# Optimization experiments

Hardware: AMD Instinct MI355X
Metric: run time of the kernel (lower is better)

## Reference

```python
import jax, jax.numpy as jnp
import numpy as np

TOP_K = 8  # config.top_k


def setup_inputs() -> dict:
    key = jax.random.key(0)
    k1, k2 = jax.random.split(key)
    B, S, H, E = 4, 4096, 4096, 64
    x = jax.random.normal(k1, (B, S, H), dtype=jnp.float32)
    # nn.Linear(hidden_size, expert_num, bias=False) weight: [E, H]
    W = jax.random.normal(k2, (E, H), dtype=jnp.float32) / np.sqrt(H).astype(np.float32)
    return {"x": x, "W": W}


def reference(x, W):
    # gate linear: [B,S,H] @ [E,H]^T -> [B,S,E]
    logits = jnp.einsum('bsh,eh->bse', x, W)
    # top-k along experts
    topk_vals, indices = jax.lax.top_k(logits, TOP_K)  # [B,S,K]
    # scatter topk values into a -inf-filled tensor. Since the scattered src
    # values are exactly the logits at those indices, this equals masking.
    E = logits.shape[-1]
    mask = jax.nn.one_hot(indices, E, dtype=bool).any(axis=-2)  # [B,S,E]
    sparse_logits = jnp.where(mask, logits, -jnp.inf)
    sparse_probs = jax.nn.softmax(sparse_logits, axis=-1)  # [B,S,E]
    gate_logit = logits.reshape(-1, E)  # [B*S, E]
    return sparse_probs, indices, gate_logit
```

## Files before the change

### kernel.cpp

```cpp
#include <hip/hip_runtime.h>
#include <math.h>

#define H_DIM  4096
#define E_NUM  64
#define N_TOK  16384
#define TPB    64
#define KC     64
#define NCHUNK (H_DIM / KC)
#define TOPK   8

#define N_PROBS  (N_TOK * E_NUM)
#define N_IDX    (N_TOK * TOPK)
#define OFF_IDX  N_PROBS
#define OFF_GATE (N_PROBS + N_IDX)


typedef __attribute__((ext_vector_type(8))) __fp16 half8;
typedef __attribute__((ext_vector_type(2))) __fp16 half2t;
typedef __attribute__((ext_vector_type(16))) float f32x16;
typedef __attribute__((ext_vector_type(4))) unsigned int uint4v;

#define XSCALE 64.0f
#define WSCALE 256.0f
#define DESCALE (1.0 / 16384.0)

__global__ __launch_bounds__(256, 1)
void gating_kernel(const float* __restrict__ x, const float* __restrict__ W,
                   float* __restrict__ out) {
  __shared__ union __align__(16) {
    struct { float xs[4][64][KC]; float ws[4][64][KC]; } t;
    float lg[TPB][E_NUM + 1];
  } u;

  const int tid  = threadIdx.x;
  const int tok0 = blockIdx.x * TPB;
  const int lane = tid & 63;
  const int wid  = tid >> 6;
  const int wm   = wid >> 1;
  const int wn   = wid & 1;
  const int l31  = lane & 31;
  const int arow = 32 * wm + l31;
  const int brow = 32 * wn + l31;
  const int khalf = 32 * (lane >> 5);

  const float* xg = x + (size_t)tok0 * H_DIM;

  auto stage = [&](const float* gbase, float* lds, int cbyte) {
#pragma unroll
    for (int i = 0; i < 4; ++i) {
      const int I   = wid * 4 + i;
      const int row = 4 * I + (lane >> 4);
      const int inrow = (lane & 15) * 16;
      const char* src = (const char*)(gbase + (size_t)row * H_DIM) + cbyte
                        + (inrow ^ ((row & 7) << 4));
      __builtin_amdgcn_global_load_lds(
          (const __attribute__((address_space(1))) unsigned int*)src,
          (__attribute__((address_space(3))) unsigned int*)((char*)lds + I * 1024),
          16, 0, 0);
    }
  };

  auto frag16 = [&](const float* base, int row, int q) -> float4 {
    return *(const float4*)((const char*)base + row * 256
                            + (q ^ ((row & 7) << 4)));
  };

  auto split8 = [&](float4 v0, float4 v1, float scale, half8& hi, half8& lo) {
    const float f[8] = {v0.x, v0.y, v0.z, v0.w, v1.x, v1.y, v1.z, v1.w};
    unsigned hu[4], lu[4];
#pragma unroll
    for (int i = 0; i < 4; ++i) {
      const float a = f[2 * i] * scale;
      const float b = f[2 * i + 1] * scale;
      half2t h = __builtin_amdgcn_cvt_pkrtz(a, b);
      const float r0 = a - (float)h.x;
      const float r1 = b - (float)h.y;
      half2t l = __builtin_amdgcn_cvt_pkrtz(r0, r1);
      hu[i] = __builtin_bit_cast(unsigned, h);
      lu[i] = __builtin_bit_cast(unsigned, l);
    }
    hi = __builtin_bit_cast(half8, (uint4v){hu[0], hu[1], hu[2], hu[3]});
    lo = __builtin_bit_cast(half8, (uint4v){lu[0], lu[1], lu[2], lu[3]});
  };

  stage(xg, &u.t.xs[0][0][0], 0);
  stage(W,  &u.t.ws[0][0][0], 0);
  stage(xg, &u.t.xs[1][0][0], KC * 4);
  stage(W,  &u.t.ws[1][0][0], KC * 4);

  f32x16 aH, aL;
  double accd[16];
#pragma unroll
  for (int r = 0; r < 16; ++r) { aH[r] = 0.f; aL[r] = 0.f; accd[r] = 0.0; }

  for (int c = 0; c < NCHUNK; ++c) {
    if (c + 2 < NCHUNK) {
      const int nb = (c + 2) & 3;
      const int cb = (c + 2) * KC * 4;
      stage(xg, &u.t.xs[nb][0][0], cb);
      stage(W,  &u.t.ws[nb][0][0], cb);
    }
    if (c + 2 < NCHUNK)      asm volatile("s_waitcnt vmcnt(16)" ::: "memory");
    else if (c + 1 < NCHUNK) asm volatile("s_waitcnt vmcnt(8)"  ::: "memory");
    else                     asm volatile("s_waitcnt vmcnt(0)"  ::: "memory");
    __builtin_amdgcn_s_barrier();
    asm volatile("" ::: "memory");

    const int b = c & 3;
    const float* xt = &u.t.xs[b][0][0];
    const float* wt = &u.t.ws[b][0][0];

#pragma unroll
    for (int kt = 0; kt < 4; ++kt) {
      const int q = kt * 64 + khalf;
      half8 ah, al, bh, bl;
      split8(frag16(xt, arow, q), frag16(xt, arow, q + 16), XSCALE, ah, al);
      split8(frag16(wt, brow, q), frag16(wt, brow, q + 16), WSCALE, bh, bl);
      aH = __builtin_amdgcn_mfma_f32_32x32x16_f16(ah, bh, aH, 0, 0, 0);
      aL = __builtin_amdgcn_mfma_f32_32x32x16_f16(al, bh, aL, 0, 0, 0);
      aH = __builtin_amdgcn_mfma_f32_32x32x16_f16(ah, bl, aH, 0, 0, 0);
      aL = __builtin_amdgcn_mfma_f32_32x32x16_f16(al, bl, aL, 0, 0, 0);
    }

    if (c & 1) {
#pragma unroll
      for (int r = 0; r < 16; ++r) {
        accd[r] += (double)aH[r] + (double)aL[r];
        aH[r] = 0.f; aL[r] = 0.f;
      }
    }
  }
  __syncthreads();

  const int rb = 4 * (lane >> 5);
  float* gate = out + OFF_GATE;
#pragma unroll
  for (int q = 0; q < 4; ++q)
#pragma unroll
    for (int j = 0; j < 4; ++j) {
      const int reg   = 4 * q + j;
      const int row32 = j + 8 * q + rb;
      const float v   = (float)(accd[reg] * DESCALE);
      const int trow  = 32 * wm + row32;
      const int e     = 32 * wn + l31;
      gate[(size_t)(tok0 + trow) * E_NUM + e] = v;
      u.lg[trow][e] = v;
    }
  __syncthreads();

  if (tid < TPB) {
    const int t = tid;
    float vals[TOPK];
    int   idxs[TOPK];
#pragma unroll
    for (int p = 0; p < TOPK; ++p) {
      float best = -INFINITY;
      int   bi   = 0;
      for (int e = 0; e < E_NUM; ++e) {
        const float v = u.lg[t][e];
        if (v > best) { best = v; bi = e; }
      }
      vals[p] = best;
      idxs[p] = bi;
      u.lg[t][bi] = -INFINITY;
    }
    const float m = vals[0];
    float s = 0.f, pr[TOPK];
#pragma unroll
    for (int p = 0; p < TOPK; ++p) { pr[p] = __expf(vals[p] - m); s += pr[p]; }
    const float inv = 1.0f / s;
    for (int e = 0; e < E_NUM; ++e) u.lg[t][e] = 0.f;
#pragma unroll
    for (int p = 0; p < TOPK; ++p) u.lg[t][idxs[p]] = pr[p] * inv;

    float* oidx = out + OFF_IDX + (size_t)(tok0 + t) * TOPK;
#pragma unroll
    for (int p = 0; p < TOPK; ++p) oidx[p] = (float)idxs[p];
  }
  __syncthreads();

  float* oprob = out + (size_t)tok0 * E_NUM;
#pragma unroll
  for (int p = 0; p < 16; ++p) {
    const int f = tid + 256 * p;
    oprob[f] = u.lg[f >> 6][f & 63];
  }
}

extern "C" void kernel_launch(void* const* d_in, const int* in_sizes, int n_in,
                              void* d_out, int out_size, void* d_ws, size_t ws_size,
                              hipStream_t stream) {
  const float* x = (const float*)d_in[0];
  const float* W = (const float*)d_in[1];
  float* out = (float*)d_out;
  dim3 grid(N_TOK / TPB);
  dim3 block(256);
  gating_kernel<<<grid, block, 0, stream>>>(x, W, out);
}
```

Baseline: 401.7 us.

## Split GEMM along K into two blocks per token tile and add reduce/epilogue kernel

Splits the hidden dimension in half so each 64-token tile is computed by two blocks. Partial results go to the gate and prob output regions, and a second kernel sums them, runs top-k and softmax, and writes the outputs. The LDS chunk shrinks to 32 and launch bounds allow 2 blocks per CU, aiming for more parallelism and occupancy to hide memory latency (512 blocks instead of 256). The cost is a second launch, an extra round trip of partial logits through global memory, and a change in summation order.

```diff
diff --git a/kernel.cpp b/kernel.cpp
--- a/kernel.cpp
+++ b/kernel.cpp
@@ -1,13 +1,15 @@
 #include <hip/hip_runtime.h>
 #include <math.h>
 
-#define H_DIM  4096
-#define E_NUM  64
-#define N_TOK  16384
-#define TPB    64
-#define KC     64
-#define NCHUNK (H_DIM / KC)
-#define TOPK   8
+#define H_DIM   4096
+#define E_NUM   64
+#define N_TOK   16384
+#define TPB     64
+#define KSPLIT  2
+#define KHALF   (H_DIM / KSPLIT)
+#define KC      32
+#define NCHUNK  (KHALF / KC)
+#define TOPK    8
 
 #define N_PROBS  (N_TOK * E_NUM)
 #define N_IDX    (N_TOK * TOPK)
@@ -24,33 +26,35 @@
 #define WSCALE 256.0f
 #define DESCALE (1.0 / 16384.0)
 
-__global__ __launch_bounds__(256, 1)
-void gating_kernel(const float* __restrict__ x, const float* __restrict__ W,
-                   float* __restrict__ out) {
-  __shared__ union __align__(16) {
-    struct { float xs[4][64][KC]; float ws[4][64][KC]; } t;
-    float lg[TPB][E_NUM + 1];
+__global__ __launch_bounds__(256, 2)
+void gemm_part(const float* __restrict__ x, const float* __restrict__ W,
+               float* __restrict__ out) {
+  __shared__ struct __align__(16) {
+    float xs[4][64][KC]; float ws[4][64][KC];
   } u;
 
-  const int tid  = threadIdx.x;
-  const int tok0 = blockIdx.x * TPB;
-  const int lane = tid & 63;
-  const int wid  = tid >> 6;
-  const int wm   = wid >> 1;
-  const int wn   = wid & 1;
-  const int l31  = lane & 31;
-  const int arow = 32 * wm + l31;
-  const int brow = 32 * wn + l31;
-  const int khalf = 32 * (lane >> 5);
-
-  const float* xg = x + (size_t)tok0 * H_DIM;
+  const int tid    = threadIdx.x;
+  const int tokgrp = blockIdx.x >> 1;
+  const int kpart  = blockIdx.x & 1;
+  const int tok0   = tokgrp * TPB;
+  const int lane   = tid & 63;
+  const int wid    = tid >> 6;
+  const int wm     = wid >> 1;
+  const int wn     = wid & 1;
+  const int l31    = lane & 31;
+  const int arow   = 32 * wm + l31;
+  const int brow   = 32 * wn + l31;
+  const int khalf  = 32 * (lane >> 5);
+
+  const float* xg = x + (size_t)tok0 * H_DIM + (size_t)kpart * KHALF;
+  const float* wg = W + (size_t)kpart * KHALF;
 
   auto stage = [&](const float* gbase, float* lds, int cbyte) {
 #pragma unroll
-    for (int i = 0; i < 4; ++i) {
-      const int I   = wid * 4 + i;
-      const int row = 4 * I + (lane >> 4);
-      const int inrow = (lane & 15) * 16;
+    for (int i = 0; i < 2; ++i) {
+      const int I     = wid * 2 + i;
+      const int row   = 8 * I + (lane >> 3);
+      const int inrow = (lane & 7) * 16;
       const char* src = (const char*)(gbase + (size_t)row * H_DIM) + cbyte
                         + (inrow ^ ((row & 7) << 4));
       __builtin_amdgcn_global_load_lds(
@@ -61,7 +65,7 @@
   };
 
   auto frag16 = [&](const float* base, int row, int q) -> float4 {
-    return *(const float4*)((const char*)base + row * 256
+    return *(const float4*)((const char*)base + row * 128
                             + (q ^ ((row & 7) << 4)));
   };
 
@@ -83,10 +87,10 @@
     lo = __builtin_bit_cast(half8, (uint4v){lu[0], lu[1], lu[2], lu[3]});
   };
 
-  stage(xg, &u.t.xs[0][0][0], 0);
-  stage(W,  &u.t.ws[0][0][0], 0);
-  stage(xg, &u.t.xs[1][0][0], KC * 4);
-  stage(W,  &u.t.ws[1][0][0], KC * 4);
+  stage(xg, &u.xs[0][0][0], 0);
+  stage(wg, &u.ws[0][0][0], 0);
+  stage(xg, &u.xs[1][0][0], KC * 4);
+  stage(wg, &u.ws[1][0][0], KC * 4);
 
   f32x16 aH, aL;
   double accd[16];
@@ -97,21 +101,21 @@
     if (c + 2 < NCHUNK) {
       const int nb = (c + 2) & 3;
       const int cb = (c + 2) * KC * 4;
-      stage(xg, &u.t.xs[nb][0][0], cb);
-      stage(W,  &u.t.ws[nb][0][0], cb);
-    }
-    if (c + 2 < NCHUNK)      asm volatile("s_waitcnt vmcnt(16)" ::: "memory");
-    else if (c + 1 < NCHUNK) asm volatile("s_waitcnt vmcnt(8)"  ::: "memory");
-    else                     asm volatile("s_waitcnt vmcnt(0)"  ::: "memory");
+      stage(xg, &u.xs[nb][0][0], cb);
+      stage(wg, &u.ws[nb][0][0], cb);
+    }
+    if (c + 2 < NCHUNK)      asm volatile("s_waitcnt vmcnt(8)" ::: "memory");
+    else if (c + 1 < NCHUNK) asm volatile("s_waitcnt vmcnt(4)" ::: "memory");
+    else                     asm volatile("s_waitcnt vmcnt(0)" ::: "memory");
     __builtin_amdgcn_s_barrier();
     asm volatile("" ::: "memory");
 
     const int b = c & 3;
-    const float* xt = &u.t.xs[b][0][0];
-    const float* wt = &u.t.ws[b][0][0];
-
-#pragma unroll
-    for (int kt = 0; kt < 4; ++kt) {
+    const float* xt = &u.xs[b][0][0];
+    const float* wt = &u.ws[b][0][0];
+
+#pragma unroll
+    for (int kt = 0; kt < 2; ++kt) {
       const int q = kt * 64 + khalf;
       half8 ah, al, bh, bl;
       split8(frag16(xt, arow, q), frag16(xt, arow, q + 16), XSCALE, ah, al);
@@ -130,10 +134,9 @@
       }
     }
   }
-  __syncthreads();
 
   const int rb = 4 * (lane >> 5);
-  float* gate = out + OFF_GATE;
+  float* pout = out + (kpart ? 0 : OFF_GATE);
 #pragma unroll
   for (int q = 0; q < 4; ++q)
 #pragma unroll
@@ -143,12 +146,38 @@
       const float v   = (float)(accd[reg] * DESCALE);
       const int trow  = 32 * wm + row32;
       const int e     = 32 * wn + l31;
-      gate[(size_t)(tok0 + trow) * E_NUM + e] = v;
-      u.lg[trow][e] = v;
-    }
+      pout[(size_t)(tok0 + trow) * E_NUM + e] = v;
+    }
+}
+
+__global__ __launch_bounds__(256, 1)
+void reduce_epilogue(float* __restrict__ out) {
+  __shared__ float lg[64][E_NUM + 1];
+
+  const int tid  = threadIdx.x;
+  const int tok0 = blockIdx.x * 64;
+  const int tx   = tid & 15;
+  const int ty   = tid >> 4;
+
+  float* gate = out + OFF_GATE;
+  float* prob = out;
+
+#pragma unroll
+  for (int i = 0; i < 4; ++i) {
+    const int t = 4 * ty + i;
+    const size_t off = (size_t)(tok0 + t) * E_NUM + 4 * tx;
+    const float4 pa = *(const float4*)(gate + off);
+    const float4 pb = *(const float4*)(prob + off);
+    float4 v = make_float4(pa.x + pb.x, pa.y + pb.y, pa.z + pb.z, pa.w + pb.w);
+    *(float4*)(gate + off) = v;
+    lg[t][4 * tx + 0] = v.x;
+    lg[t][4 * tx + 1] = v.y;
+    lg[t][4 * tx + 2] = v.z;
+    lg[t][4 * tx + 3] = v.w;
+  }
   __syncthreads();
 
-  if (tid < TPB) {
+  if (tid < 64) {
     const int t = tid;
     float vals[TOPK];
     int   idxs[TOPK];
@@ -157,21 +186,21 @@
       float best = -INFINITY;
       int   bi   = 0;
       for (int e = 0; e < E_NUM; ++e) {
-        const float v = u.lg[t][e];
+        const float v = lg[t][e];
         if (v > best) { best = v; bi = e; }
       }
       vals[p] = best;
       idxs[p] = bi;
-      u.lg[t][bi] = -INFINITY;
+      lg[t][bi] = -INFINITY;
     }
     const float m = vals[0];
     float s = 0.f, pr[TOPK];
 #pragma unroll
     for (int p = 0; p < TOPK; ++p) { pr[p] = __expf(vals[p] - m); s += pr[p]; }
     const float inv = 1.0f / s;
-    for (int e = 0; e < E_NUM; ++e) u.lg[t][e] = 0.f;
-#pragma unroll
-    for (int p = 0; p < TOPK; ++p) u.lg[t][idxs[p]] = pr[p] * inv;
+    for (int e = 0; e < E_NUM; ++e) lg[t][e] = 0.f;
+#pragma unroll
+    for (int p = 0; p < TOPK; ++p) lg[t][idxs[p]] = pr[p] * inv;
 
     float* oidx = out + OFF_IDX + (size_t)(tok0 + t) * TOPK;
 #pragma unroll
@@ -179,11 +208,11 @@
   }
   __syncthreads();
 
-  float* oprob = out + (size_t)tok0 * E_NUM;
+  float* oprob = prob + (size_t)tok0 * E_NUM;
 #pragma unroll
   for (int p = 0; p < 16; ++p) {
     const int f = tid + 256 * p;
-    oprob[f] = u.lg[f >> 6][f & 63];
+    oprob[f] = lg[f >> 6][f & 63];
   }
 }
 
@@ -193,7 +222,6 @@
   const float* x = (const float*)d_in[0];
   const float* W = (const float*)d_in[1];
   float* out = (float*)d_out;
-  dim3 grid(N_TOK / TPB);
-  dim3 block(256);
-  gating_kernel<<<grid, block, 0, stream>>>(x, W, out);
+  gemm_part<<<dim3(N_TOK / TPB * KSPLIT), dim3(256), 0, stream>>>(x, W, out);
+  reduce_epilogue<<<dim3(N_TOK / 64), dim3(256), 0, stream>>>(out);
 }
```

After: 395.4 us. Within noise of the previous version (-1.6%).
